# Performance work log

Hardware: AMD Instinct MI355X
Metric: run time of the kernel (lower is better)

The kernel has to match this reference:

```python
import jax, jax.numpy as jnp
import numpy as np

DIM = 2048
N_HEADS = 16
N_KV = 4
HEAD_DIM = DIM // N_HEADS  # 128
B, S = 2, 2048
EPS = float(np.finfo(np.float32).eps)  # torch RMSNorm eps=None -> finfo eps


def _rotate_half(x):
    # interleaved-pair rotation: out[..., ::2] = -x[..., 1::2]; out[..., 1::2] = x[..., ::2]
    x2 = x.reshape(x.shape[:-1] + (HEAD_DIM // 2, 2))
    rot = jnp.stack([-x2[..., 1], x2[..., 0]], axis=-1)
    return rot.reshape(x.shape)


def _rmsnorm(x, w):
    var = jnp.mean(x * x, axis=-1, keepdims=True)
    return x * jax.lax.rsqrt(var + EPS) * w


def setup_inputs() -> dict:
    key = jax.random.key(0)
    ks = jax.random.split(key, 5)
    out_f = (N_HEADS + 2 * N_KV) * HEAD_DIM  # 3072
    return {
        "x": jax.random.normal(ks[0], (B, S, DIM), jnp.float32),
        "wqkv": jax.random.normal(ks[1], (out_f, DIM), jnp.float32) * (2.0 / (DIM + out_f)) ** 0.5,
        "wo": jax.random.normal(ks[2], (DIM, DIM), jnp.float32) * (1.0 / DIM) ** 0.5,
        "q_norm_w": jnp.ones((HEAD_DIM,), jnp.float32),
        "k_norm_w": jnp.ones((HEAD_DIM,), jnp.float32),
        "freqs_cos": jnp.cos(jax.random.normal(ks[3], (S, 1, HEAD_DIM), jnp.float32)),
        "freqs_sin": jnp.sin(jax.random.normal(ks[4], (S, 1, HEAD_DIM), jnp.float32)),
    }


def reference(x, wqkv, wo, q_norm_w, k_norm_w, freqs_cos, freqs_sin):
    b, s, _ = x.shape
    qkv = jnp.einsum("bsd,od->bso", x, wqkv)
    q_size = N_HEADS * HEAD_DIM
    kv_size = N_KV * HEAD_DIM
    xq = qkv[..., :q_size].reshape(b, s, N_HEADS, HEAD_DIM)
    xk = qkv[..., q_size:q_size + kv_size].reshape(b, s, N_KV, HEAD_DIM)
    xv = qkv[..., q_size + kv_size:].reshape(b, s, N_KV, HEAD_DIM)
    xq = _rmsnorm(xq, q_norm_w)
    xk = _rmsnorm(xk, k_norm_w)
    # RoPE (freqs broadcast over batch and heads)
    xq = xq * freqs_cos + _rotate_half(xq) * freqs_sin
    xk = xk * freqs_cos + _rotate_half(xk) * freqs_sin
    # GQA: group query heads per kv head instead of materializing repeats
    rep = N_HEADS // N_KV
    q = xq.transpose(0, 2, 1, 3).reshape(b, N_KV, rep, s, HEAD_DIM)
    k = xk.transpose(0, 2, 1, 3)  # [b, kv, s, d]
    v = xv.transpose(0, 2, 1, 3)
    scale = 1.0 / jnp.sqrt(jnp.asarray(HEAD_DIM, x.dtype))
    scores = jnp.einsum("bhgqd,bhkd->bhgqk", q, k) * scale
    probs = jax.nn.softmax(scores, axis=-1)
    attn = jnp.einsum("bhgqk,bhkd->bhgqd", probs, v)
    attn = attn.reshape(b, N_HEADS, s, HEAD_DIM).transpose(0, 2, 1, 3).reshape(b, s, DIM)
    return jnp.einsum("bsd,od->bso", attn, wo)
```

## Files before the change

### kernel.cpp

```cpp
#include <hip/hip_runtime.h>
#include <hip/hip_bf16.h>

typedef unsigned short u16;
typedef __bf16 bf16x8 __attribute__((ext_vector_type(8)));
typedef __bf16 bf16x4 __attribute__((ext_vector_type(4)));
typedef u16 u16x8 __attribute__((ext_vector_type(8)));
typedef float f32x4 __attribute__((ext_vector_type(4)));
typedef float f32x16 __attribute__((ext_vector_type(16)));

__device__ __forceinline__ u16 f2bf(float f) {
    unsigned u = __float_as_uint(f);
    return (u16)((u + 0x7fffu + ((u >> 16) & 1u)) >> 16);
}
__device__ __forceinline__ unsigned pkbf2(float a, float b) {
    __hip_bfloat162 h = __float22bfloat162_rn(make_float2(a, b));
    return *(unsigned*)&h;
}

__device__ __forceinline__ void gload16(const u16* g, u16* l) {
    __builtin_amdgcn_global_load_lds(
        (const __attribute__((address_space(1))) void*)g,
        (__attribute__((address_space(3))) void*)l, 16, 0, 0);
}

__global__ void cvt_bf16(const float* __restrict__ src, u16* __restrict__ dst, int n4) {
    int i = blockIdx.x * 256 + threadIdx.x;
    if (i >= n4) return;
    float4 v = *(const float4*)(src + (size_t)i * 4);
    uint2 o; o.x = pkbf2(v.x, v.y); o.y = pkbf2(v.z, v.w);
    *(uint2*)(dst + (size_t)i * 4) = o;
}

__device__ __forceinline__ void gemm_core(const u16* __restrict__ Ab,
                                          const u16* __restrict__ Bb, int K,
                                          f32x4 acc[4][4], int wave, int lane) {
    __shared__ u16 As[2][128 * 32];
    __shared__ u16 Bs[2][128 * 32];
    const int quad = lane >> 4, l16 = lane & 15;
    const int wr = (wave >> 1) * 64, wc = (wave & 1) * 64;

    const int srow = lane >> 2;
    const int selem = (lane & 3) * 8;
    const u16* ga = Ab + (size_t)(wave * 32 + srow) * K + selem;
    const u16* gb = Bb + (size_t)(wave * 32 + srow) * K + selem;
    const size_t rstep = (size_t)16 * K;
    u16* la0A[2] = { &As[0][(wave * 32) * 32], &As[1][(wave * 32) * 32] };
    u16* la1A[2] = { &As[0][(wave * 32 + 16) * 32], &As[1][(wave * 32 + 16) * 32] };
    u16* la0B[2] = { &Bs[0][(wave * 32) * 32], &Bs[1][(wave * 32) * 32] };
    u16* la1B[2] = { &Bs[0][(wave * 32 + 16) * 32], &Bs[1][(wave * 32 + 16) * 32] };

    gload16(ga,         la0A[0]);
    gload16(ga + rstep, la1A[0]);
    gload16(gb,         la0B[0]);
    gload16(gb + rstep, la1B[0]);
    __syncthreads();

    const int nk = K >> 5;
    for (int kt = 0; kt < nk; ++kt) {
        const int cur = kt & 1, nxt = cur ^ 1;
        if (kt + 1 < nk) {
            const int off = (kt + 1) * 32;
            gload16(ga + off,         la0A[nxt]);
            gload16(ga + off + rstep, la1A[nxt]);
            gload16(gb + off,         la0B[nxt]);
            gload16(gb + off + rstep, la1B[nxt]);
        }
        bf16x8 af[4], bfr[4];
#pragma unroll
        for (int mt = 0; mt < 4; ++mt)
            af[mt] = *(const bf16x8*)&As[cur][(wr + mt * 16 + l16) * 32 + quad * 8];
#pragma unroll
        for (int nt = 0; nt < 4; ++nt)
            bfr[nt] = *(const bf16x8*)&Bs[cur][(wc + nt * 16 + l16) * 32 + quad * 8];
#pragma unroll
        for (int mt = 0; mt < 4; ++mt)
#pragma unroll
            for (int nt = 0; nt < 4; ++nt)
                acc[mt][nt] = __builtin_amdgcn_mfma_f32_16x16x32_bf16(
                    af[mt], bfr[nt], acc[mt][nt], 0, 0, 0);
        __syncthreads();
    }
}

__global__ __launch_bounds__(256)
void gemm_bt(const u16* __restrict__ A, const u16* __restrict__ B,
             float* __restrict__ C, int M, int N, int K) {
    const int tid = threadIdx.x, wave = tid >> 6, lane = tid & 63;
    const int quad = lane >> 4, l16 = lane & 15;
    const int wr = (wave >> 1) * 64, wc = (wave & 1) * 64;
    const size_t bm = (size_t)blockIdx.y * 128, bn = (size_t)blockIdx.x * 128;
    f32x4 acc[4][4] = {};
    gemm_core(A + bm * K, B + bn * K, K, acc, wave, lane);
#pragma unroll
    for (int mt = 0; mt < 4; ++mt)
#pragma unroll
        for (int nt = 0; nt < 4; ++nt)
#pragma unroll
            for (int r = 0; r < 4; ++r)
                C[(bm + wr + mt * 16 + quad * 4 + r) * (size_t)N + bn + wc + nt * 16 + l16] =
                    acc[mt][nt][r];
}

__global__ __launch_bounds__(256)
void gemm_qkv(const u16* __restrict__ xb, const u16* __restrict__ wq,
              const float* __restrict__ qw, const float* __restrict__ kw,
              const float* __restrict__ fcos, const float* __restrict__ fsin,
              u16* __restrict__ qb, u16* __restrict__ kb, u16* __restrict__ vt) {
    const int tid = threadIdx.x, wave = tid >> 6, lane = tid & 63;
    const int quad = lane >> 4, l16 = lane & 15;
    const int wr = (wave >> 1) * 64, wc = (wave & 1) * 64;
    const int tn = blockIdx.x, bmb = blockIdx.y;
    f32x4 acc[4][4] = {};
    gemm_core(xb + (size_t)bmb * 128 * 2048, wq + (size_t)tn * 128 * 2048, 2048,
              acc, wave, lane);

    const int b = bmb >> 4;
    const int sbase = (bmb & 15) * 128 + wr;

    if (tn >= 20) {
        const int kv = tn - 20;
        u16* base = vt + (size_t)(b * 4 + kv) * 128 * 2048;
#pragma unroll
        for (int mt = 0; mt < 4; ++mt) {
            int s0 = sbase + mt * 16 + quad * 4;
#pragma unroll
            for (int nt = 0; nt < 4; ++nt) {
                int col = wc + nt * 16 + l16;
                bf16x4 pv;
#pragma unroll
                for (int r = 0; r < 4; ++r) pv[r] = (__bf16)acc[mt][nt][r];
                *(bf16x4*)(base + (size_t)col * 2048 + s0) = pv;
            }
        }
        return;
    }

    __shared__ float red[2][128];
    float ssq[4][4];
#pragma unroll
    for (int mt = 0; mt < 4; ++mt)
#pragma unroll
        for (int r = 0; r < 4; ++r) {
            float t = 0.f;
#pragma unroll
            for (int nt = 0; nt < 4; ++nt) t += acc[mt][nt][r] * acc[mt][nt][r];
#pragma unroll
            for (int off = 1; off <= 8; off <<= 1) t += __shfl_xor(t, off);
            ssq[mt][r] = t;
        }
    if (l16 == 0)
#pragma unroll
        for (int mt = 0; mt < 4; ++mt)
#pragma unroll
            for (int r = 0; r < 4; ++r)
                red[wave & 1][wr + mt * 16 + quad * 4 + r] = ssq[mt][r];
    __syncthreads();

    const float qscl = (tn < 16) ? 0.08838834764831845f * 1.4426950408889634f : 1.0f;
    const float* wp = (tn < 16) ? qw : kw;
    float wcol[4];
#pragma unroll
    for (int nt = 0; nt < 4; ++nt) wcol[nt] = wp[wc + nt * 16 + l16];
    u16* dstbase = (tn < 16) ? qb + (size_t)(b * 16 + tn) * 2048 * 128
                             : kb + (size_t)(b * 4 + (tn - 16)) * 2048 * 128;
    const float sgn = (l16 & 1) ? 1.f : -1.f;

#pragma unroll
    for (int mt = 0; mt < 4; ++mt) {
#pragma unroll
        for (int r = 0; r < 4; ++r) {
            int row = wr + mt * 16 + quad * 4 + r;
            float var = (red[0][row] + red[1][row]) * (1.0f / 128.0f);
            float rms = rsqrtf(var + 1.1920928955078125e-07f) * qscl;
            int s = sbase + mt * 16 + quad * 4 + r;
            const float* fc = fcos + (size_t)s * 128 + wc;
            const float* fn = fsin + (size_t)s * 128 + wc;
            u16* drow = dstbase + (size_t)s * 128 + wc;
#pragma unroll
            for (int nt = 0; nt < 4; ++nt) {
                float y = acc[mt][nt][r] * rms * wcol[nt];
                float yp = __shfl_xor(y, 1);
                float o = y * fc[nt * 16 + l16] + sgn * yp * fn[nt * 16 + l16];
                drow[nt * 16 + l16] = f2bf(o);
            }
        }
    }
}

#define KBUF(c) ((c) * 8192)
#define VBUF(c) (16384 + (c) * 8192)
__global__ __launch_bounds__(256, 2)
void flash_attn(const u16* __restrict__ qb, const u16* __restrict__ kb,
                const u16* __restrict__ vt, u16* __restrict__ ab) {
    __shared__ u16 smem[32768];
    __shared__ float Llds[128];

    const int tid = threadIdx.x;
    const int wave = tid >> 6, lane = tid & 63;
    const int hf = lane >> 5, c32 = lane & 31;
    const int qt = blockIdx.x, hh = blockIdx.y, bb = blockIdx.z;
    const int kh = hh >> 2;

    const u16* Qbase = qb + (size_t)(bb * 16 + hh) * 2048 * 128;
    const u16* Kbase = kb + (size_t)(bb * 4 + kh) * 2048 * 128;
    const u16* Vbase = vt + (size_t)(bb * 4 + kh) * 128 * 2048;

    bf16x8 aq[8];
#pragma unroll
    for (int kq = 0; kq < 8; ++kq)
        aq[kq] = *(const bf16x8*)(Qbase +
            (size_t)(qt * 128 + wave * 32 + c32) * 128 + kq * 16 + hf * 8);

    f32x16 O[4] = {};
    float lacc = 0.f;

    const int st_key = tid >> 4, st_c16 = tid & 15;
    const int st_d = tid >> 3, st_c8 = tid & 7;

    u16x8 kreg[4], vreg[4];
#pragma unroll
    for (int it = 0; it < 4; ++it) {
        int key = st_key + it * 16, d = st_d + it * 32;
        kreg[it] = *(const u16x8*)(Kbase + (size_t)key * 128 + st_c16 * 8);
        vreg[it] = *(const u16x8*)(Vbase + (size_t)d * 2048 + st_c8 * 8);
    }
#pragma unroll
    for (int it = 0; it < 4; ++it) {
        int key = st_key + it * 16, d = st_d + it * 32;
        *(u16x8*)&smem[KBUF(0) + key * 128 + ((st_c16 ^ (key & 7)) * 8)] = kreg[it];
        *(u16x8*)&smem[VBUF(0) + d * 64 + ((st_c8 ^ (d & 7)) * 8)] = vreg[it];
    }
    __syncthreads();

    for (int kt = 0; kt < 32; ++kt) {
        const int cur = kt & 1, nxt = cur ^ 1;
        if (kt < 31) {
            const int key0n = (kt + 1) * 64;
#pragma unroll
            for (int it = 0; it < 4; ++it) {
                int key = st_key + it * 16, d = st_d + it * 32;
                kreg[it] = *(const u16x8*)(Kbase + (size_t)(key0n + key) * 128 + st_c16 * 8);
                vreg[it] = *(const u16x8*)(Vbase + (size_t)d * 2048 + key0n + st_c8 * 8);
            }
        }

        f32x16 sc[2] = {};
#pragma unroll
        for (int kq = 0; kq < 8; ++kq) {
#pragma unroll
            for (int mt = 0; mt < 2; ++mt) {
                bf16x8 kf = *(const bf16x8*)&smem[KBUF(cur) + (mt * 32 + c32) * 128 +
                                                 (((kq * 2 + hf) ^ (c32 & 7)) * 8)];
                sc[mt] = __builtin_amdgcn_mfma_f32_32x32x16_bf16(kf, aq[kq], sc[mt], 0, 0, 0);
            }
        }

        int pdw[2][8];
#pragma unroll
        for (int mt = 0; mt < 2; ++mt) {
            float p[16];
#pragma unroll
            for (int r = 0; r < 16; ++r) {
                p[r] = __builtin_amdgcn_exp2f(sc[mt][r]);
                lacc += p[r];
            }
#pragma unroll
            for (int i = 0; i < 8; ++i) pdw[mt][i] = (int)pkbf2(p[2 * i], p[2 * i + 1]);
        }

        if (kt < 31) {
#pragma unroll
            for (int it = 0; it < 4; ++it) {
                int key = st_key + it * 16, d = st_d + it * 32;
                *(u16x8*)&smem[KBUF(nxt) + key * 128 + ((st_c16 ^ (key & 7)) * 8)] = kreg[it];
                *(u16x8*)&smem[VBUF(nxt) + d * 64 + ((st_c8 ^ (d & 7)) * 8)] = vreg[it];
            }
        }

#pragma unroll
        for (int kc = 0; kc < 4; ++kc) {
            const int mt = kc >> 1, L = kc & 1;
            int s0 = hf ? pdw[mt][4 * L + 0] : pdw[mt][4 * L + 2];
            int s1 = hf ? pdw[mt][4 * L + 1] : pdw[mt][4 * L + 3];
            int r0 = __shfl_xor(s0, 32);
            int r1 = __shfl_xor(s1, 32);
            union { int i[4]; bf16x8 v; } u;
            u.i[0] = hf ? r0 : pdw[mt][4 * L + 0];
            u.i[1] = hf ? r1 : pdw[mt][4 * L + 1];
            u.i[2] = hf ? pdw[mt][4 * L + 2] : r0;
            u.i[3] = hf ? pdw[mt][4 * L + 3] : r1;
#pragma unroll
            for (int dt = 0; dt < 4; ++dt) {
                bf16x8 vf = *(const bf16x8*)&smem[VBUF(cur) + (dt * 32 + c32) * 64 +
                                                 (((kc * 2 + hf) ^ (c32 & 7)) * 8)];
                O[dt] = __builtin_amdgcn_mfma_f32_32x32x16_bf16(u.v, vf, O[dt], 0, 0, 0);
            }
        }
        __syncthreads();
    }

    float l = lacc + __shfl_xor(lacc, 32);
    if (hf == 0) Llds[wave * 32 + c32] = l;

    float inv[16];
#pragma unroll
    for (int r = 0; r < 16; ++r)
        inv[r] = __builtin_amdgcn_rcpf(Llds[wave * 32 + (r & 3) + 8 * (r >> 2) + 4 * hf]);

    u16* scr = &smem[wave * 32 * 136];
#pragma unroll
    for (int dt = 0; dt < 4; ++dt)
#pragma unroll
        for (int r = 0; r < 16; ++r) {
            int q_r = (r & 3) + 8 * (r >> 2) + 4 * hf;
            scr[q_r * 136 + dt * 32 + c32] = f2bf(O[dt][r] * inv[r]);
        }
#pragma unroll
    for (int it = 0; it < 8; ++it) {
        int f = it * 64 + lane;
        int row = f >> 4, c = f & 15;
        u16x8 v = *(const u16x8*)&scr[row * 136 + c * 8];
        int qg = qt * 128 + wave * 32 + row;
        *(u16x8*)(ab + ((size_t)(bb * 2048 + qg)) * 2048 + hh * 128 + c * 8) = v;
    }
}

extern "C" void kernel_launch(void* const* d_in, const int* in_sizes, int n_in,
                              void* d_out, int out_size, void* d_ws, size_t ws_size,
                              hipStream_t stream) {
    const float* x    = (const float*)d_in[0];
    const float* wqkv = (const float*)d_in[1];
    const float* wo   = (const float*)d_in[2];
    const float* qw   = (const float*)d_in[3];
    const float* kw   = (const float*)d_in[4];
    const float* fc   = (const float*)d_in[5];
    const float* fs   = (const float*)d_in[6];
    float* out = (float*)d_out;
    char* ws = (char*)d_ws;

    u16* xb    = (u16*)(ws + 0);
    u16* wqkvb = (u16*)(ws + 16777216);
    u16* wob   = (u16*)(ws + 29360128);
    u16* qb    = (u16*)(ws + 37748736);
    u16* kb    = (u16*)(ws + 54525952);
    u16* vt    = (u16*)(ws + 58720256);
    u16* ab    = (u16*)(ws + 62914560);

    cvt_bf16<<<8192, 256, 0, stream>>>(x, xb, 2097152);
    cvt_bf16<<<6144, 256, 0, stream>>>(wqkv, wqkvb, 1572864);
    cvt_bf16<<<4096, 256, 0, stream>>>(wo, wob, 1048576);
    gemm_qkv<<<dim3(24, 32), 256, 0, stream>>>(xb, wqkvb, qw, kw, fc, fs, qb, kb, vt);
    flash_attn<<<dim3(16, 16, 2), 256, 0, stream>>>(qb, kb, vt, ab);
    gemm_bt<<<dim3(16, 32), 256, 0, stream>>>(ab, wob, out, 4096, 2048, 2048);
}
```

Measured before the change: 336.8 us.

## Rewrite GEMM core with larger tiles, BK=64, swizzled LDS, and 8-wave blocks

```diff
diff --git a/kernel.cpp b/kernel.cpp
--- a/kernel.cpp
+++ b/kernel.cpp
@@ -23,6 +23,17 @@
         (__attribute__((address_space(3))) void*)l, 16, 0, 0);
 }
 
+__device__ __forceinline__ void block_sync() {
+    __builtin_amdgcn_sched_barrier(0);
+    __builtin_amdgcn_s_barrier();
+    __builtin_amdgcn_sched_barrier(0);
+}
+template<int N> __device__ __forceinline__ void waitvm() {
+    if constexpr (N == 0)      asm volatile("s_waitcnt vmcnt(0)" ::: "memory");
+    else if constexpr (N == 6) asm volatile("s_waitcnt vmcnt(6)" ::: "memory");
+    else                       asm volatile("s_waitcnt vmcnt(8)" ::: "memory");
+}
+
 __global__ void cvt_bf16(const float* __restrict__ src, u16* __restrict__ dst, int n4) {
     int i = blockIdx.x * 256 + threadIdx.x;
     if (i >= n4) return;
@@ -31,157 +42,187 @@
     *(uint2*)(dst + (size_t)i * 4) = o;
 }
 
-__device__ __forceinline__ void gemm_core(const u16* __restrict__ Ab,
-                                          const u16* __restrict__ Bb, int K,
-                                          f32x4 acc[4][4], int wave, int lane) {
-    __shared__ u16 As[2][128 * 32];
-    __shared__ u16 Bs[2][128 * 32];
+template<int ROWS>
+__device__ __forceinline__ void stage_tile(const u16* __restrict__ g, int K,
+                                           int k0, u16* l, int tid) {
+#pragma unroll
+    for (int s = 0; s < ROWS / 64; ++s) {
+        int row = s * 64 + (tid >> 3);
+        int sc = (tid & 7) ^ ((tid >> 3) & 7);
+        gload16(g + (size_t)row * K + k0 + sc * 8, l + s * 4096 + tid * 8);
+    }
+}
+
+template<int BM, int BN>
+__device__ __forceinline__ void gemm_pipeline(const u16* __restrict__ Ab,
+                                              const u16* __restrict__ Bb, int K,
+                                              u16* sAll,
+                                              f32x4 (&acc)[BM / 32][BN / 64],
+                                              int tid) {
+    constexpr int MR = BM / 32, NR = BN / 64;
+    constexpr int TILE = (BM + BN) * 64;
+    const int lane = tid & 63, wave = tid >> 6;
     const int quad = lane >> 4, l16 = lane & 15;
-    const int wr = (wave >> 1) * 64, wc = (wave & 1) * 64;
-
-    const int srow = lane >> 2;
-    const int selem = (lane & 3) * 8;
-    const u16* ga = Ab + (size_t)(wave * 32 + srow) * K + selem;
-    const u16* gb = Bb + (size_t)(wave * 32 + srow) * K + selem;
-    const size_t rstep = (size_t)16 * K;
-    u16* la0A[2] = { &As[0][(wave * 32) * 32], &As[1][(wave * 32) * 32] };
-    u16* la1A[2] = { &As[0][(wave * 32 + 16) * 32], &As[1][(wave * 32 + 16) * 32] };
-    u16* la0B[2] = { &Bs[0][(wave * 32) * 32], &Bs[1][(wave * 32) * 32] };
-    u16* la1B[2] = { &Bs[0][(wave * 32 + 16) * 32], &Bs[1][(wave * 32 + 16) * 32] };
-
-    gload16(ga,         la0A[0]);
-    gload16(ga + rstep, la1A[0]);
-    gload16(gb,         la0B[0]);
-    gload16(gb + rstep, la1B[0]);
-    __syncthreads();
-
-    const int nk = K >> 5;
-    for (int kt = 0; kt < nk; ++kt) {
-        const int cur = kt & 1, nxt = cur ^ 1;
-        if (kt + 1 < nk) {
-            const int off = (kt + 1) * 32;
-            gload16(ga + off,         la0A[nxt]);
-            gload16(ga + off + rstep, la1A[nxt]);
-            gload16(gb + off,         la0B[nxt]);
-            gload16(gb + off + rstep, la1B[nxt]);
-        }
-        bf16x8 af[4], bfr[4];
-#pragma unroll
-        for (int mt = 0; mt < 4; ++mt)
-            af[mt] = *(const bf16x8*)&As[cur][(wr + mt * 16 + l16) * 32 + quad * 8];
-#pragma unroll
-        for (int nt = 0; nt < 4; ++nt)
-            bfr[nt] = *(const bf16x8*)&Bs[cur][(wc + nt * 16 + l16) * 32 + quad * 8];
-#pragma unroll
-        for (int mt = 0; mt < 4; ++mt)
-#pragma unroll
-            for (int nt = 0; nt < 4; ++nt)
-                acc[mt][nt] = __builtin_amdgcn_mfma_f32_16x16x32_bf16(
-                    af[mt], bfr[nt], acc[mt][nt], 0, 0, 0);
-        __syncthreads();
-    }
-}
-
-__global__ __launch_bounds__(256)
+    const int wm = wave >> 2, wn = wave & 3;
+    const int ar0 = wm * (BM / 2) + l16;
+    const int br0 = wn * (BN / 4) + l16;
+
+    u16* sA0 = sAll;        u16* sB0 = sAll + BM * 64;
+    u16* sA1 = sAll + TILE; u16* sB1 = sAll + TILE + BM * 64;
+
+    stage_tile<BM>(Ab, K, 0, sA0, tid);
+    stage_tile<BN>(Bb, K, 0, sB0, tid);
+
+    const int nt = K >> 6;
+    for (int t = 0; t < nt; ++t) {
+        const u16* cA = (t & 1) ? sA1 : sA0;
+        const u16* cB = (t & 1) ? sB1 : sB0;
+        if (t + 1 < nt) {
+            u16* nA = (t & 1) ? sA0 : sA1;
+            u16* nB = (t & 1) ? sB0 : sB1;
+            stage_tile<BM>(Ab, K, (t + 1) * 64, nA, tid);
+            stage_tile<BN>(Bb, K, (t + 1) * 64, nB, tid);
+            waitvm<(BM + BN) / 64>();
+        } else {
+            waitvm<0>();
+        }
+        block_sync();
+#pragma unroll
+        for (int kk = 0; kk < 2; ++kk) {
+            const int c = kk * 4 + quad;
+            bf16x8 af[MR], bf[NR];
+#pragma unroll
+            for (int m = 0; m < MR; ++m) {
+                int r = ar0 + m * 16;
+                af[m] = *(const bf16x8*)&cA[r * 64 + ((c ^ (r & 7)) * 8)];
+            }
+#pragma unroll
+            for (int n = 0; n < NR; ++n) {
+                int r = br0 + n * 16;
+                bf[n] = *(const bf16x8*)&cB[r * 64 + ((c ^ (r & 7)) * 8)];
+            }
+            __builtin_amdgcn_s_setprio(1);
+#pragma unroll
+            for (int m = 0; m < MR; ++m)
+#pragma unroll
+                for (int n = 0; n < NR; ++n)
+                    acc[m][n] = __builtin_amdgcn_mfma_f32_16x16x32_bf16(
+                        af[m], bf[n], acc[m][n], 0, 0, 0);
+            __builtin_amdgcn_s_setprio(0);
+        }
+        block_sync();
+    }
+}
+
+__global__ __launch_bounds__(512, 2)
 void gemm_bt(const u16* __restrict__ A, const u16* __restrict__ B,
              float* __restrict__ C, int M, int N, int K) {
-    const int tid = threadIdx.x, wave = tid >> 6, lane = tid & 63;
+    __shared__ u16 sAll[2 * (128 + 256) * 64];
+    const int tid = threadIdx.x;
+    const int wave = tid >> 6, lane = tid & 63;
     const int quad = lane >> 4, l16 = lane & 15;
-    const int wr = (wave >> 1) * 64, wc = (wave & 1) * 64;
-    const size_t bm = (size_t)blockIdx.y * 128, bn = (size_t)blockIdx.x * 128;
+    const int wm = wave >> 2, wn = wave & 3;
+    const size_t bm = (size_t)blockIdx.y * 128, bn = (size_t)blockIdx.x * 256;
     f32x4 acc[4][4] = {};
-    gemm_core(A + bm * K, B + bn * K, K, acc, wave, lane);
-#pragma unroll
-    for (int mt = 0; mt < 4; ++mt)
-#pragma unroll
-        for (int nt = 0; nt < 4; ++nt)
+    gemm_pipeline<128, 256>(A + bm * K, B + bn * K, K, sAll, acc, tid);
+#pragma unroll
+    for (int m = 0; m < 4; ++m)
+#pragma unroll
+        for (int n = 0; n < 4; ++n)
 #pragma unroll
             for (int r = 0; r < 4; ++r)
-                C[(bm + wr + mt * 16 + quad * 4 + r) * (size_t)N + bn + wc + nt * 16 + l16] =
-                    acc[mt][nt][r];
-}
-
-__global__ __launch_bounds__(256)
+                C[(bm + wm * 64 + m * 16 + quad * 4 + r) * (size_t)N +
+                  bn + wn * 64 + n * 16 + l16] = acc[m][n][r];
+}
+
+__global__ __launch_bounds__(512, 2)
 void gemm_qkv(const u16* __restrict__ xb, const u16* __restrict__ wq,
               const float* __restrict__ qw, const float* __restrict__ kw,
               const float* __restrict__ fcos, const float* __restrict__ fsin,
               u16* __restrict__ qb, u16* __restrict__ kb, u16* __restrict__ vt) {
-    const int tid = threadIdx.x, wave = tid >> 6, lane = tid & 63;
+    __shared__ u16 sAll[2 * (256 + 256) * 64];
+    const int tid = threadIdx.x;
+    const int wave = tid >> 6, lane = tid & 63;
     const int quad = lane >> 4, l16 = lane & 15;
-    const int wr = (wave >> 1) * 64, wc = (wave & 1) * 64;
-    const int tn = blockIdx.x, bmb = blockIdx.y;
-    f32x4 acc[4][4] = {};
-    gemm_core(xb + (size_t)bmb * 128 * 2048, wq + (size_t)tn * 128 * 2048, 2048,
-              acc, wave, lane);
-
-    const int b = bmb >> 4;
-    const int sbase = (bmb & 15) * 128 + wr;
-
-    if (tn >= 20) {
-        const int kv = tn - 20;
-        u16* base = vt + (size_t)(b * 4 + kv) * 128 * 2048;
-#pragma unroll
-        for (int mt = 0; mt < 4; ++mt) {
-            int s0 = sbase + mt * 16 + quad * 4;
-#pragma unroll
-            for (int nt = 0; nt < 4; ++nt) {
-                int col = wc + nt * 16 + l16;
+    const int wm = wave >> 2, wn = wave & 3;
+    const int bx = blockIdx.x, by = blockIdx.y;
+    f32x4 acc[8][4] = {};
+    gemm_pipeline<256, 256>(xb + (size_t)by * 256 * 2048,
+                            wq + (size_t)bx * 256 * 2048, 2048, sAll, acc, tid);
+
+    const int b = by >> 3;
+    const int sb = (by & 7) * 256 + wm * 128;
+    const int headh = wn >> 1;
+    const int dcol0 = (wn & 1) * 64;
+
+    if (bx >= 10) {
+        const int kvh = (bx - 10) * 2 + headh;
+        u16* base = vt + (size_t)(b * 4 + kvh) * 128 * 2048;
+#pragma unroll
+        for (int m = 0; m < 8; ++m) {
+            int s0 = sb + m * 16 + quad * 4;
+#pragma unroll
+            for (int n = 0; n < 4; ++n) {
+                int d = dcol0 + n * 16 + l16;
                 bf16x4 pv;
 #pragma unroll
-                for (int r = 0; r < 4; ++r) pv[r] = (__bf16)acc[mt][nt][r];
-                *(bf16x4*)(base + (size_t)col * 2048 + s0) = pv;
+                for (int r = 0; r < 4; ++r) pv[r] = (__bf16)acc[m][n][r];
+                *(bf16x4*)(base + (size_t)d * 2048 + s0) = pv;
             }
         }
         return;
     }
 
-    __shared__ float red[2][128];
-    float ssq[4][4];
-#pragma unroll
-    for (int mt = 0; mt < 4; ++mt)
+    float* red = (float*)sAll;
+    float ssq[8][4];
+#pragma unroll
+    for (int m = 0; m < 8; ++m)
 #pragma unroll
         for (int r = 0; r < 4; ++r) {
             float t = 0.f;
 #pragma unroll
-            for (int nt = 0; nt < 4; ++nt) t += acc[mt][nt][r] * acc[mt][nt][r];
+            for (int n = 0; n < 4; ++n) t += acc[m][n][r] * acc[m][n][r];
 #pragma unroll
             for (int off = 1; off <= 8; off <<= 1) t += __shfl_xor(t, off);
-            ssq[mt][r] = t;
+            ssq[m][r] = t;
         }
     if (l16 == 0)
 #pragma unroll
-        for (int mt = 0; mt < 4; ++mt)
+        for (int m = 0; m < 8; ++m)
 #pragma unroll
             for (int r = 0; r < 4; ++r)
-                red[wave & 1][wr + mt * 16 + quad * 4 + r] = ssq[mt][r];
+                red[((wn & 1) * 2 + headh) * 256 + wm * 128 + m * 16 + quad * 4 + r] =
+                    ssq[m][r];
     __syncthreads();
 
-    const float qscl = (tn < 16) ? 0.08838834764831845f * 1.4426950408889634f : 1.0f;
-    const float* wp = (tn < 16) ? qw : kw;
+    const bool isQ = bx < 8;
+    const float qscl = isQ ? 0.08838834764831845f * 1.4426950408889634f : 1.0f;
+    const float* wp = isQ ? qw : kw;
     float wcol[4];
 #pragma unroll
-    for (int nt = 0; nt < 4; ++nt) wcol[nt] = wp[wc + nt * 16 + l16];
-    u16* dstbase = (tn < 16) ? qb + (size_t)(b * 16 + tn) * 2048 * 128
-                             : kb + (size_t)(b * 4 + (tn - 16)) * 2048 * 128;
+    for (int n = 0; n < 4; ++n) wcol[n] = wp[dcol0 + n * 16 + l16];
+    u16* dstbase = isQ ? qb + (size_t)(b * 16 + bx * 2 + headh) * 2048 * 128
+                       : kb + (size_t)(b * 4 + (bx - 8) * 2 + headh) * 2048 * 128;
     const float sgn = (l16 & 1) ? 1.f : -1.f;
 
 #pragma unroll
-    for (int mt = 0; mt < 4; ++mt) {
+    for (int m = 0; m < 8; ++m) {
 #pragma unroll
         for (int r = 0; r < 4; ++r) {
-            int row = wr + mt * 16 + quad * 4 + r;
-            float var = (red[0][row] + red[1][row]) * (1.0f / 128.0f);
+            int rowl = wm * 128 + m * 16 + quad * 4 + r;
+            float var = (red[(0 + headh) * 256 + rowl] +
+                         red[(2 + headh) * 256 + rowl]) * (1.0f / 128.0f);
             float rms = rsqrtf(var + 1.1920928955078125e-07f) * qscl;
-            int s = sbase + mt * 16 + quad * 4 + r;
-            const float* fc = fcos + (size_t)s * 128 + wc;
-            const float* fn = fsin + (size_t)s * 128 + wc;
-            u16* drow = dstbase + (size_t)s * 128 + wc;
-#pragma unroll
-            for (int nt = 0; nt < 4; ++nt) {
-                float y = acc[mt][nt][r] * rms * wcol[nt];
+            int s = sb + m * 16 + quad * 4 + r;
+            const float* fc = fcos + (size_t)s * 128 + dcol0;
+            const float* fn = fsin + (size_t)s * 128 + dcol0;
+            u16* drow = dstbase + (size_t)s * 128 + dcol0;
+#pragma unroll
+            for (int n = 0; n < 4; ++n) {
+                float y = acc[m][n][r] * rms * wcol[n];
                 float yp = __shfl_xor(y, 1);
-                float o = y * fc[nt * 16 + l16] + sgn * yp * fn[nt * 16 + l16];
-                drow[nt * 16 + l16] = f2bf(o);
+                float o = y * fc[n * 16 + l16] + sgn * yp * fn[n * 16 + l16];
+                drow[n * 16 + l16] = f2bf(o);
             }
         }
     }
@@ -349,7 +390,7 @@
     cvt_bf16<<<8192, 256, 0, stream>>>(x, xb, 2097152);
     cvt_bf16<<<6144, 256, 0, stream>>>(wqkv, wqkvb, 1572864);
     cvt_bf16<<<4096, 256, 0, stream>>>(wo, wob, 1048576);
-    gemm_qkv<<<dim3(24, 32), 256, 0, stream>>>(xb, wqkvb, qw, kw, fc, fs, qb, kb, vt);
+    gemm_qkv<<<dim3(12, 16), 512, 0, stream>>>(xb, wqkvb, qw, kw, fc, fs, qb, kb, vt);
     flash_attn<<<dim3(16, 16, 2), 256, 0, stream>>>(qb, kb, vt, ab);
-    gemm_bt<<<dim3(16, 32), 256, 0, stream>>>(ab, wob, out, 4096, 2048, 2048);
-}
+    gemm_bt<<<dim3(8, 32), 512, 0, stream>>>(ab, wob, out, 4096, 2048, 2048);
+}
```

Result: faster. 317.0 us (-5.9%).
